# Performance work log

Measured on AMD Instinct MI355X. Metric: run time of the kernel, lower is better.

The kernel has to match this reference:

```python
import jax, jax.numpy as jnp
import numpy as np

N_WIRES = 8
DIM = 1 << N_WIRES  # 256

# Precompute CNOT permutations (torchquantum convention: wire 0 = MSB)
_idx = np.arange(DIM)
_CNOT_PERMS = []
for _c in range(N_WIRES):
    _t = (_c + 1) % N_WIRES
    _cbit = (_idx >> (N_WIRES - 1 - _c)) & 1
    _CNOT_PERMS.append(np.where(_cbit == 1, _idx ^ (1 << (N_WIRES - 1 - _t)), _idx))
# PauliZ signs per wire: [DIM, N_WIRES]
_ZSIGNS = np.stack([1.0 - 2.0 * ((_idx >> (N_WIRES - 1 - w)) & 1) for w in range(N_WIRES)], axis=1).astype(np.float32)


def _quantum_heads(x, theta):
    """x: [B,S,H,8] angles; theta: [8]. Returns PauliZ expectations [B,S,H,8].

    Simulates per (token,head) an 8-qubit circuit: RX(x_i+theta_i) on wire i
    (encoder RX followed by trainable RX on same wire = one RX with summed angle),
    then CNOT ring 0->1..6->7, 7->0, then MeasureAll PauliZ.
    """
    B, S, H, _ = x.shape
    N = B * S * H
    ang = x.reshape(N, N_WIRES) + theta  # [N,8]
    state = jnp.zeros((N, DIM), dtype=jnp.complex64).at[:, 0].set(1.0)
    half = ang * 0.5
    c_all = jnp.cos(half)
    s_all = jnp.sin(half)
    for w in range(N_WIRES):
        A = 1 << w
        Bdim = 1 << (N_WIRES - 1 - w)
        s = state.reshape(N, A, 2, Bdim)
        a0, a1 = s[:, :, 0, :], s[:, :, 1, :]
        c = c_all[:, w][:, None, None].astype(jnp.complex64)
        isn = (1j * s_all[:, w][:, None, None]).astype(jnp.complex64)
        n0 = c * a0 - isn * a1
        n1 = -isn * a0 + c * a1
        state = jnp.stack([n0, n1], axis=2).reshape(N, DIM)
    for perm in _CNOT_PERMS:
        state = state[:, perm]
    probs = state.real ** 2 + state.imag ** 2  # [N,256]
    exp = probs @ jnp.asarray(_ZSIGNS)  # [N,8]
    return exp.reshape(B, S, H, N_WIRES)


def _mha(proj, W_combine, num_heads):
    # proj: [B,S,E]; q = k = v = proj (identical deterministic projections)
    B, S, E = proj.shape
    d_k = E // num_heads
    qkv = proj.reshape(B, S, num_heads, d_k).transpose(0, 2, 1, 3)  # [B,H,S,dk]
    scores = jnp.einsum('bhqd,bhkd->bhqk', qkv, qkv) / jnp.sqrt(jnp.float32(d_k))
    attn = jax.nn.softmax(scores, axis=-1)
    out = jnp.einsum('bhqk,bhkd->bhqd', attn, qkv)
    out = out.transpose(0, 2, 1, 3).reshape(B, S, E)
    return out @ W_combine.T


def setup_inputs() -> dict:
    key = jax.random.key(0)
    k1, k2, k3 = jax.random.split(key, 3)
    B, S, H = 8, 1024, 8
    E = H * N_WIRES  # 64
    x = jax.random.normal(k1, (B, S, E), dtype=jnp.float32)
    theta = jax.random.normal(k2, (N_WIRES,), dtype=jnp.float32)
    W_combine = jax.random.normal(k3, (E, E), dtype=jnp.float32) * (1.0 / np.sqrt(E))
    return {'x': x, 'theta': theta, 'W_combine': W_combine}


def reference(x, theta, W_combine):
    B, S, E = x.shape
    H = E // N_WIRES
    proj = _quantum_heads(x.reshape(B, S, H, N_WIRES), theta).reshape(B, S, E)
    return _mha(proj, W_combine, H)
```

## Files before the change

kernel.cpp:

```cpp
#include <hip/hip_runtime.h>

typedef _Float16 half4v __attribute__((ext_vector_type(4)));
typedef float float4v __attribute__((ext_vector_type(4)));

#define NW 8
#define S_ 1024
#define H_ 8
#define B_ 8
#define BH 64
#define NROW 8192
#define E_ 64
#define KST 20

__global__ __launch_bounds__(256, 4) void attn_kernel(
        const float* __restrict__ x, const float* __restrict__ theta,
        float* __restrict__ attnout) {
    __shared__ _Float16 kvh[S_ * KST];
    int bh = blockIdx.x;
    int b = bh >> 3, h = bh & 7;
    int tid = threadIdx.x;

    float th[8];
#pragma unroll
    for (int i = 0; i < 8; ++i) th[i] = theta[i];

    if (tid < 8) kvh[8 + tid] = (tid == 0) ? (_Float16)1.0f : (_Float16)0.0f;

    for (int s = tid; s < S_; s += 256) {
        const float4* xp = (const float4*)(x + (((size_t)(b << 10) + s) << 6) + (h << 3));
        float4 x0 = xp[0];
        float4 x1 = xp[1];
        float c0 = __cosf(x0.x + th[0]);
        float c1 = __cosf(x0.y + th[1]);
        float c2 = __cosf(x0.z + th[2]);
        float c3 = __cosf(x0.w + th[3]);
        float c4 = __cosf(x1.x + th[4]);
        float c5 = __cosf(x1.y + th[5]);
        float c6 = __cosf(x1.z + th[6]);
        float c7 = __cosf(x1.w + th[7]);
        float e1 = c0 * c1;
        float e2 = e1 * c2;
        float e3 = e2 * c3;
        float e4 = e3 * c4;
        float e5 = e4 * c5;
        float e6 = e5 * c6;
        float e7 = e6 * c7;
        float e0 = ((c1 * c2) * (c3 * c4)) * ((c5 * c6) * c7);
        half4v lo = {(_Float16)e0, (_Float16)e1, (_Float16)e2, (_Float16)e3};
        half4v hi = {(_Float16)e4, (_Float16)e5, (_Float16)e6, (_Float16)e7};
        *(half4v*)&kvh[s * KST]     = lo;
        *(half4v*)&kvh[s * KST + 4] = hi;
    }
    __syncthreads();

    int lane = tid & 63;
    int wv   = tid >> 6;
    int col  = lane & 15;
    int quad = lane >> 4;
    int q0   = blockIdx.y * 64 + wv * 16;

    int qidx = (quad < 2) ? ((q0 + col) * KST + quad * 4) : 12;
    half4v qf = *(const half4v*)&kvh[qidx];
    qf *= (_Float16)0.51012921f;

    int kaddr = (quad < 2) ? (col * KST + quad * 4) : 12;
    int kstep = (quad < 2) ? (16 * KST) : 0;

    int va    = (col < 8) ? (quad * 4 * KST + col) : col;
    int vstep = (col < 8) ? (16 * KST) : 0;
    int vr    = (col < 8) ? KST : 0;

    float4v oacc = {0.f, 0.f, 0.f, 0.f};
    const float4v zc = {0.f, 0.f, 0.f, 0.f};
    const float SH = 4.08040428f;

    for (int kt = 0; kt < 64; ++kt) {
        half4v kf = *(const half4v*)&kvh[kaddr];
        float4v st = __builtin_amdgcn_mfma_f32_16x16x16f16(kf, qf, zc, 0, 0, 0);
        _Float16 p0 = (_Float16)exp2f(st[0] - SH);
        _Float16 p1 = (_Float16)exp2f(st[1] - SH);
        _Float16 p2 = (_Float16)exp2f(st[2] - SH);
        _Float16 p3 = (_Float16)exp2f(st[3] - SH);
        half4v pf = {p0, p1, p2, p3};
        _Float16 v0 = kvh[va];
        _Float16 v1 = kvh[va + vr];
        _Float16 v2 = kvh[va + 2 * vr];
        _Float16 v3 = kvh[va + 3 * vr];
        half4v vf = {v0, v1, v2, v3};
        oacc = __builtin_amdgcn_mfma_f32_16x16x16f16(pf, vf, oacc, 0, 0, 0);
        kaddr += kstep;
        va += vstep;
    }

    int lsrc = (lane & 48) | 8;
    float l0 = __shfl(oacc[0], lsrc, 64);
    float l1 = __shfl(oacc[1], lsrc, 64);
    float l2 = __shfl(oacc[2], lsrc, 64);
    float l3 = __shfl(oacc[3], lsrc, 64);
    if (col < 8) {
        float* op = attnout + (((size_t)(b << 10) + q0 + quad * 4) << 6) + (h << 3) + col;
        op[0 << 6] = oacc[0] * __builtin_amdgcn_rcpf(l0);
        op[1 << 6] = oacc[1] * __builtin_amdgcn_rcpf(l1);
        op[2 << 6] = oacc[2] * __builtin_amdgcn_rcpf(l2);
        op[3 << 6] = oacc[3] * __builtin_amdgcn_rcpf(l3);
    }
}

#define CROWS 16
__global__ __launch_bounds__(256) void combine_kernel(
        const float* __restrict__ A, const float* __restrict__ W,
        float* __restrict__ out) {
    __shared__ float wl[E_ * 65];
    __shared__ float al[CROWS][E_];
    int r0 = blockIdx.x * CROWS;

    for (int idx = threadIdx.x; idx < E_ * E_; idx += 256) {
        int e = idx >> 6, k = idx & 63;
        wl[k * 65 + e] = W[idx];
    }
    ((float4*)al)[threadIdx.x] = ((const float4*)(A + (size_t)r0 * E_))[threadIdx.x];
    __syncthreads();

    int e = threadIdx.x & 63;
    int g = threadIdx.x >> 6;
    float acc[4] = {0, 0, 0, 0};
    for (int k = 0; k < E_; ++k) {
        float wv = wl[k * 65 + e];
#pragma unroll
        for (int j = 0; j < 4; ++j) acc[j] += al[g * 4 + j][k] * wv;
    }
#pragma unroll
    for (int j = 0; j < 4; ++j) {
        int r = r0 + g * 4 + j;
        out[(size_t)r * E_ + e] = acc[j];
    }
}

extern "C" void kernel_launch(void* const* d_in, const int* in_sizes, int n_in,
                              void* d_out, int out_size, void* d_ws, size_t ws_size,
                              hipStream_t stream) {
    const float* x     = (const float*)d_in[0];
    const float* theta = (const float*)d_in[1];
    const float* W     = (const float*)d_in[2];
    float* out = (float*)d_out;

    float* attnout = (float*)d_ws;

    attn_kernel<<<dim3(BH, S_ / 64), 256, 0, stream>>>(x, theta, attnout);
    combine_kernel<<<NROW / CROWS, 256, 0, stream>>>(attnout, W, out);
}
```

Measured before the change: 87.54 us.

## Process two query tiles per wave with transposed V in LDS and prefetch

Each wave now handles 32 queries (two 16-row MFMA tiles) that share each K and V fragment load, and the grid is halved. V is stored transposed in a separate LDS buffer, so each lane reads a contiguous half4 instead of four scalar loads, and K/V fragments for the next iteration are prefetched. The goal is to cut redundant LDS traffic and the per-block K/V preprocessing, which is now done once per 128 queries instead of once per 64. In exchange LDS use grows and occupancy drops, with launch bounds lowered from 4 to 2.

```diff
diff --git a/kernel.cpp b/kernel.cpp
--- a/kernel.cpp
+++ b/kernel.cpp
@@ -11,11 +11,13 @@
 #define NROW 8192
 #define E_ 64
 #define KST 20
+#define VST 1032
 
-__global__ __launch_bounds__(256, 4) void attn_kernel(
+__global__ __launch_bounds__(256, 2) void attn_kernel(
         const float* __restrict__ x, const float* __restrict__ theta,
         float* __restrict__ attnout) {
     __shared__ _Float16 kvh[S_ * KST];
+    __shared__ _Float16 vT[16 * VST];
     int bh = blockIdx.x;
     int b = bh >> 3, h = bh & 7;
     int tid = threadIdx.x;
@@ -25,6 +27,16 @@
     for (int i = 0; i < 8; ++i) th[i] = theta[i];
 
     if (tid < 8) kvh[8 + tid] = (tid == 0) ? (_Float16)1.0f : (_Float16)0.0f;
+
+    {
+        const half4v ones  = {(_Float16)1.0f, (_Float16)1.0f, (_Float16)1.0f, (_Float16)1.0f};
+        const half4v zeros = {(_Float16)0.0f, (_Float16)0.0f, (_Float16)0.0f, (_Float16)0.0f};
+        for (int i = tid; i < 8 * (S_ / 4); i += 256) {
+            int d = 8 + (i >> 8);
+            int s4 = (i & 255) << 2;
+            *(half4v*)&vT[d * VST + s4] = (d == 8) ? ones : zeros;
+        }
+    }
 
     for (int s = tid; s < S_; s += 256) {
         const float4* xp = (const float4*)(x + (((size_t)(b << 10) + s) << 6) + (h << 3));
@@ -46,10 +58,16 @@
         float e6 = e5 * c6;
         float e7 = e6 * c7;
         float e0 = ((c1 * c2) * (c3 * c4)) * ((c5 * c6) * c7);
-        half4v lo = {(_Float16)e0, (_Float16)e1, (_Float16)e2, (_Float16)e3};
-        half4v hi = {(_Float16)e4, (_Float16)e5, (_Float16)e6, (_Float16)e7};
+        _Float16 h0 = (_Float16)e0, h1 = (_Float16)e1, h2 = (_Float16)e2, h3 = (_Float16)e3;
+        _Float16 h4 = (_Float16)e4, h5 = (_Float16)e5, h6 = (_Float16)e6, h7 = (_Float16)e7;
+        half4v lo = {h0, h1, h2, h3};
+        half4v hi = {h4, h5, h6, h7};
         *(half4v*)&kvh[s * KST]     = lo;
         *(half4v*)&kvh[s * KST + 4] = hi;
+        vT[0 * VST + s] = h0; vT[1 * VST + s] = h1;
+        vT[2 * VST + s] = h2; vT[3 * VST + s] = h3;
+        vT[4 * VST + s] = h4; vT[5 * VST + s] = h5;
+        vT[6 * VST + s] = h6; vT[7 * VST + s] = h7;
     }
     __syncthreads();
 
@@ -57,52 +75,70 @@
     int wv   = tid >> 6;
     int col  = lane & 15;
     int quad = lane >> 4;
-    int q0   = blockIdx.y * 64 + wv * 16;
+    int q0   = blockIdx.y * 128 + wv * 32;
 
-    int qidx = (quad < 2) ? ((q0 + col) * KST + quad * 4) : 12;
-    half4v qf = *(const half4v*)&kvh[qidx];
-    qf *= (_Float16)0.51012921f;
+    int qia = (quad < 2) ? ((q0 + col) * KST + quad * 4) : 12;
+    int qib = (quad < 2) ? ((q0 + 16 + col) * KST + quad * 4) : 12;
+    half4v qfa = *(const half4v*)&kvh[qia];
+    half4v qfb = *(const half4v*)&kvh[qib];
+    qfa *= (_Float16)0.51012921f;
+    qfb *= (_Float16)0.51012921f;
 
-    int kaddr = (quad < 2) ? (col * KST + quad * 4) : 12;
+    int kbase = (quad < 2) ? (col * KST + quad * 4) : 12;
     int kstep = (quad < 2) ? (16 * KST) : 0;
+    int vbase = col * VST + quad * 4;
 
-    int va    = (col < 8) ? (quad * 4 * KST + col) : col;
-    int vstep = (col < 8) ? (16 * KST) : 0;
-    int vr    = (col < 8) ? KST : 0;
-
-    float4v oacc = {0.f, 0.f, 0.f, 0.f};
+    float4v oa = {0.f, 0.f, 0.f, 0.f};
+    float4v ob = {0.f, 0.f, 0.f, 0.f};
     const float4v zc = {0.f, 0.f, 0.f, 0.f};
     const float SH = 4.08040428f;
 
+    half4v kf = *(const half4v*)&kvh[kbase];
+    half4v vf = *(const half4v*)&vT[vbase];
+
+#pragma unroll 2
     for (int kt = 0; kt < 64; ++kt) {
-        half4v kf = *(const half4v*)&kvh[kaddr];
-        float4v st = __builtin_amdgcn_mfma_f32_16x16x16f16(kf, qf, zc, 0, 0, 0);
-        _Float16 p0 = (_Float16)exp2f(st[0] - SH);
-        _Float16 p1 = (_Float16)exp2f(st[1] - SH);
-        _Float16 p2 = (_Float16)exp2f(st[2] - SH);
-        _Float16 p3 = (_Float16)exp2f(st[3] - SH);
-        half4v pf = {p0, p1, p2, p3};
-        _Float16 v0 = kvh[va];
-        _Float16 v1 = kvh[va + vr];
-        _Float16 v2 = kvh[va + 2 * vr];
-        _Float16 v3 = kvh[va + 3 * vr];
-        half4v vf = {v0, v1, v2, v3};
-        oacc = __builtin_amdgcn_mfma_f32_16x16x16f16(pf, vf, oacc, 0, 0, 0);
-        kaddr += kstep;
-        va += vstep;
+        float4v sa = __builtin_amdgcn_mfma_f32_16x16x16f16(kf, qfa, zc, 0, 0, 0);
+        float4v sb = __builtin_amdgcn_mfma_f32_16x16x16f16(kf, qfb, zc, 0, 0, 0);
+        int nkt = (kt + 1) & 63;
+        half4v kfn = *(const half4v*)&kvh[kbase + nkt * kstep];
+        half4v vfn = *(const half4v*)&vT[vbase + nkt * 16];
+        half4v pa = {(_Float16)exp2f(sa[0] - SH), (_Float16)exp2f(sa[1] - SH),
+                     (_Float16)exp2f(sa[2] - SH), (_Float16)exp2f(sa[3] - SH)};
+        half4v pb = {(_Float16)exp2f(sb[0] - SH), (_Float16)exp2f(sb[1] - SH),
+                     (_Float16)exp2f(sb[2] - SH), (_Float16)exp2f(sb[3] - SH)};
+        oa = __builtin_amdgcn_mfma_f32_16x16x16f16(pa, vf, oa, 0, 0, 0);
+        ob = __builtin_amdgcn_mfma_f32_16x16x16f16(pb, vf, ob, 0, 0, 0);
+        kf = kfn;
+        vf = vfn;
     }
 
     int lsrc = (lane & 48) | 8;
-    float l0 = __shfl(oacc[0], lsrc, 64);
-    float l1 = __shfl(oacc[1], lsrc, 64);
-    float l2 = __shfl(oacc[2], lsrc, 64);
-    float l3 = __shfl(oacc[3], lsrc, 64);
-    if (col < 8) {
-        float* op = attnout + (((size_t)(b << 10) + q0 + quad * 4) << 6) + (h << 3) + col;
-        op[0 << 6] = oacc[0] * __builtin_amdgcn_rcpf(l0);
-        op[1 << 6] = oacc[1] * __builtin_amdgcn_rcpf(l1);
-        op[2 << 6] = oacc[2] * __builtin_amdgcn_rcpf(l2);
-        op[3 << 6] = oacc[3] * __builtin_amdgcn_rcpf(l3);
+    {
+        float l0 = __shfl(oa[0], lsrc, 64);
+        float l1 = __shfl(oa[1], lsrc, 64);
+        float l2 = __shfl(oa[2], lsrc, 64);
+        float l3 = __shfl(oa[3], lsrc, 64);
+        if (col < 8) {
+            float* op = attnout + (((size_t)(b << 10) + q0 + quad * 4) << 6) + (h << 3) + col;
+            op[0 << 6] = oa[0] * __builtin_amdgcn_rcpf(l0);
+            op[1 << 6] = oa[1] * __builtin_amdgcn_rcpf(l1);
+            op[2 << 6] = oa[2] * __builtin_amdgcn_rcpf(l2);
+            op[3 << 6] = oa[3] * __builtin_amdgcn_rcpf(l3);
+        }
+    }
+    {
+        float l0 = __shfl(ob[0], lsrc, 64);
+        float l1 = __shfl(ob[1], lsrc, 64);
+        float l2 = __shfl(ob[2], lsrc, 64);
+        float l3 = __shfl(ob[3], lsrc, 64);
+        if (col < 8) {
+            float* op = attnout + (((size_t)(b << 10) + q0 + 16 + quad * 4) << 6) + (h << 3) + col;
+            op[0 << 6] = ob[0] * __builtin_amdgcn_rcpf(l0);
+            op[1 << 6] = ob[1] * __builtin_amdgcn_rcpf(l1);
+            op[2 << 6] = ob[2] * __builtin_amdgcn_rcpf(l2);
+            op[3 << 6] = ob[3] * __builtin_amdgcn_rcpf(l3);
+        }
     }
 }
 
@@ -146,6 +182,6 @@
 
     float* attnout = (float*)d_ws;
 
-    attn_kernel<<<dim3(BH, S_ / 64), 256, 0, stream>>>(x, theta, attnout);
+    attn_kernel<<<dim3(BH, S_ / 128), 256, 0, stream>>>(x, theta, attnout);
     combine_kernel<<<NROW / CROWS, 256, 0, stream>>>(attnout, W, out);
 }
```

Measured after the change: 84.53 us. 1.04x faster.

## Transpose K/V LDS layout, swap PV MFMA operands, software-pipeline key loads

Applied to the files above, without the earlier changes.

Stores the per-head features transposed in LDS (dimension-major with a padded stride) so V fragments load as contiguous half4 vectors. It also swaps the PV MFMA operand order so each lane ends up holding four output dimensions for one query, which allows a single float4 store per lane. The key loop is unrolled by two with next-iteration loads issued ahead, and uses raw exp2 plus packed RTZ fp16 conversion. This aims to cut LDS instruction count and the scalar exp/convert overhead. In exchange K fragments now need four scalar LDS reads, and the transposed writes may hit bank conflicts.

```diff
diff --git a/kernel.cpp b/kernel.cpp
--- a/kernel.cpp
+++ b/kernel.cpp
@@ -1,6 +1,7 @@
 #include <hip/hip_runtime.h>
 
 typedef _Float16 half4v __attribute__((ext_vector_type(4)));
+typedef __fp16 fp16x2 __attribute__((ext_vector_type(2)));
 typedef float float4v __attribute__((ext_vector_type(4)));
 
 #define NW 8
@@ -10,12 +11,21 @@
 #define BH 64
 #define NROW 8192
 #define E_ 64
-#define KST 20
+#define VST 1032
+#define ZOFF (9 * VST)
+#define NLDS (9 * VST + 16)
+
+static __device__ inline half4v pack4(float a, float b, float c, float d) {
+    union { fp16x2 f2[2]; half4v h4; } u;
+    u.f2[0] = __builtin_amdgcn_cvt_pkrtz(a, b);
+    u.f2[1] = __builtin_amdgcn_cvt_pkrtz(c, d);
+    return u.h4;
+}
 
 __global__ __launch_bounds__(256, 4) void attn_kernel(
         const float* __restrict__ x, const float* __restrict__ theta,
         float* __restrict__ attnout) {
-    __shared__ _Float16 kvh[S_ * KST];
+    __shared__ _Float16 vT[NLDS];
     int bh = blockIdx.x;
     int b = bh >> 3, h = bh & 7;
     int tid = threadIdx.x;
@@ -24,7 +34,12 @@
 #pragma unroll
     for (int i = 0; i < 8; ++i) th[i] = theta[i];
 
-    if (tid < 8) kvh[8 + tid] = (tid == 0) ? (_Float16)1.0f : (_Float16)0.0f;
+    {
+        const half4v zer = {(_Float16)0.f, (_Float16)0.f, (_Float16)0.f, (_Float16)0.f};
+        const half4v one = {(_Float16)1.f, (_Float16)1.f, (_Float16)1.f, (_Float16)1.f};
+        if (tid < 4) *(half4v*)&vT[ZOFF + tid * 4] = zer;
+        *(half4v*)&vT[8 * VST + tid * 4] = one;
+    }
 
     for (int s = tid; s < S_; s += 256) {
         const float4* xp = (const float4*)(x + (((size_t)(b << 10) + s) << 6) + (h << 3));
@@ -46,10 +61,14 @@
         float e6 = e5 * c6;
         float e7 = e6 * c7;
         float e0 = ((c1 * c2) * (c3 * c4)) * ((c5 * c6) * c7);
-        half4v lo = {(_Float16)e0, (_Float16)e1, (_Float16)e2, (_Float16)e3};
-        half4v hi = {(_Float16)e4, (_Float16)e5, (_Float16)e6, (_Float16)e7};
-        *(half4v*)&kvh[s * KST]     = lo;
-        *(half4v*)&kvh[s * KST + 4] = hi;
+        vT[0 * VST + s] = (_Float16)e0;
+        vT[1 * VST + s] = (_Float16)e1;
+        vT[2 * VST + s] = (_Float16)e2;
+        vT[3 * VST + s] = (_Float16)e3;
+        vT[4 * VST + s] = (_Float16)e4;
+        vT[5 * VST + s] = (_Float16)e5;
+        vT[6 * VST + s] = (_Float16)e6;
+        vT[7 * VST + s] = (_Float16)e7;
     }
     __syncthreads();
 
@@ -59,51 +78,71 @@
     int quad = lane >> 4;
     int q0   = blockIdx.y * 64 + wv * 16;
 
-    int qidx = (quad < 2) ? ((q0 + col) * KST + quad * 4) : 12;
-    half4v qf = *(const half4v*)&kvh[qidx];
-    qf *= (_Float16)0.51012921f;
+    bool lo2 = (quad < 2);
 
-    int kaddr = (quad < 2) ? (col * KST + quad * 4) : 12;
-    int kstep = (quad < 2) ? (16 * KST) : 0;
+    half4v qf;
+    {
+        int d0 = quad * 4;
+        int a0 = lo2 ? ((d0 + 0) * VST + q0 + col) : (ZOFF + 0);
+        int a1 = lo2 ? ((d0 + 1) * VST + q0 + col) : (ZOFF + 1);
+        int a2 = lo2 ? ((d0 + 2) * VST + q0 + col) : (ZOFF + 2);
+        int a3 = lo2 ? ((d0 + 3) * VST + q0 + col) : (ZOFF + 3);
+        half4v t = {vT[a0], vT[a1], vT[a2], vT[a3]};
+        qf = t * (_Float16)0.51012921f;
+    }
 
-    int va    = (col < 8) ? (quad * 4 * KST + col) : col;
-    int vstep = (col < 8) ? (16 * KST) : 0;
-    int vr    = (col < 8) ? KST : 0;
+    int rb0 = lo2 ? ((quad * 4 + 0) * VST) : (ZOFF + 0);
+    int rb1 = lo2 ? ((quad * 4 + 1) * VST) : (ZOFF + 1);
+    int rb2 = lo2 ? ((quad * 4 + 2) * VST) : (ZOFF + 2);
+    int rb3 = lo2 ? ((quad * 4 + 3) * VST) : (ZOFF + 3);
+    int cbase = lo2 ? col : 0;
+    int cstep = lo2 ? 16 : 0;
+
+    int vbase = (col < 9) ? (col * VST) : ZOFF;
+    int vstep = (col < 9) ? 16 : 0;
+
+#define LOADK(dst, t) { int c_ = cbase + (t) * cstep; \
+        half4v r_ = {vT[rb0 + c_], vT[rb1 + c_], vT[rb2 + c_], vT[rb3 + c_]}; dst = r_; }
+#define LOADV(dst, t) { dst = *(const half4v*)&vT[vbase + quad * 4 + (t) * vstep]; }
 
     float4v oacc = {0.f, 0.f, 0.f, 0.f};
     const float4v zc = {0.f, 0.f, 0.f, 0.f};
     const float SH = 4.08040428f;
 
-    for (int kt = 0; kt < 64; ++kt) {
-        half4v kf = *(const half4v*)&kvh[kaddr];
-        float4v st = __builtin_amdgcn_mfma_f32_16x16x16f16(kf, qf, zc, 0, 0, 0);
-        _Float16 p0 = (_Float16)exp2f(st[0] - SH);
-        _Float16 p1 = (_Float16)exp2f(st[1] - SH);
-        _Float16 p2 = (_Float16)exp2f(st[2] - SH);
-        _Float16 p3 = (_Float16)exp2f(st[3] - SH);
-        half4v pf = {p0, p1, p2, p3};
-        _Float16 v0 = kvh[va];
-        _Float16 v1 = kvh[va + vr];
-        _Float16 v2 = kvh[va + 2 * vr];
-        _Float16 v3 = kvh[va + 3 * vr];
-        half4v vf = {v0, v1, v2, v3};
-        oacc = __builtin_amdgcn_mfma_f32_16x16x16f16(pf, vf, oacc, 0, 0, 0);
-        kaddr += kstep;
-        va += vstep;
+    half4v kA, vA, kB, vB, kN, vN, kM, vM;
+    LOADK(kA, 0); LOADV(vA, 0);
+    LOADK(kB, 1); LOADV(vB, 1);
+
+    for (int kt = 0; kt < 64; kt += 2) {
+        float4v s0 = __builtin_amdgcn_mfma_f32_16x16x16f16(kA, qf, zc, 0, 0, 0);
+        int t2 = (kt + 2) & 63;
+        LOADK(kN, t2); LOADV(vN, t2);
+        float p0 = __builtin_amdgcn_exp2f(s0[0] - SH);
+        float p1 = __builtin_amdgcn_exp2f(s0[1] - SH);
+        float p2 = __builtin_amdgcn_exp2f(s0[2] - SH);
+        float p3 = __builtin_amdgcn_exp2f(s0[3] - SH);
+        half4v pa = pack4(p0, p1, p2, p3);
+        oacc = __builtin_amdgcn_mfma_f32_16x16x16f16(vA, pa, oacc, 0, 0, 0);
+        float4v s1 = __builtin_amdgcn_mfma_f32_16x16x16f16(kB, qf, zc, 0, 0, 0);
+        int t3 = (kt + 3) & 63;
+        LOADK(kM, t3); LOADV(vM, t3);
+        float r0 = __builtin_amdgcn_exp2f(s1[0] - SH);
+        float r1 = __builtin_amdgcn_exp2f(s1[1] - SH);
+        float r2 = __builtin_amdgcn_exp2f(s1[2] - SH);
+        float r3 = __builtin_amdgcn_exp2f(s1[3] - SH);
+        half4v pb = pack4(r0, r1, r2, r3);
+        oacc = __builtin_amdgcn_mfma_f32_16x16x16f16(vB, pb, oacc, 0, 0, 0);
+        kA = kN; vA = vN; kB = kM; vB = vM;
     }
 
-    int lsrc = (lane & 48) | 8;
-    float l0 = __shfl(oacc[0], lsrc, 64);
-    float l1 = __shfl(oacc[1], lsrc, 64);
-    float l2 = __shfl(oacc[2], lsrc, 64);
-    float l3 = __shfl(oacc[3], lsrc, 64);
-    if (col < 8) {
-        float* op = attnout + (((size_t)(b << 10) + q0 + quad * 4) << 6) + (h << 3) + col;
-        op[0 << 6] = oacc[0] * __builtin_amdgcn_rcpf(l0);
-        op[1 << 6] = oacc[1] * __builtin_amdgcn_rcpf(l1);
-        op[2 << 6] = oacc[2] * __builtin_amdgcn_rcpf(l2);
-        op[3 << 6] = oacc[3] * __builtin_amdgcn_rcpf(l3);
+    float l = __shfl(oacc[0], 32 | col, 64);
+    if (lo2) {
+        float inv = __builtin_amdgcn_rcpf(l);
+        float4 ov = make_float4(oacc[0] * inv, oacc[1] * inv, oacc[2] * inv, oacc[3] * inv);
+        *(float4*)(attnout + (((size_t)(b << 10) + q0 + col) << 6) + (h << 3) + quad * 4) = ov;
     }
+#undef LOADK
+#undef LOADV
 }
 
 #define CROWS 16
```

After: 80.74 us. -7.8%, faster.
